# Performance work log

Measured on AMD Instinct MI355X. Metric: run time of the kernel, lower is better.

Reference implementation:

```python
import jax, jax.numpy as jnp
import numpy as np

B, L, H, E, V, T = 64, 512, 512, 512, 64, 200  # L must equal H (attention broadcast in source)
SOS_TOKEN = 0


def setup_inputs() -> dict:
    key = jax.random.key(0)
    ks = jax.random.split(key, 16)
    s = 0.05
    return {
        "seq_embeddings": jax.random.normal(ks[0], (B, L, H), jnp.float32),
        "key_w": jax.random.normal(ks[1], (H, H), jnp.float32) * s,
        "key_b": jax.random.normal(ks[2], (H,), jnp.float32) * s,
        "value_w": jax.random.normal(ks[3], (H, H), jnp.float32) * s,
        "value_b": jax.random.normal(ks[4], (H,), jnp.float32) * s,
        "char_emb": jax.random.normal(ks[5], (V, E), jnp.float32) * s,
        "w_ih": jax.random.normal(ks[6], (4 * H, E + H), jnp.float32) * s,
        "w_hh": jax.random.normal(ks[7], (4 * H, H), jnp.float32) * s,
        "b_ih": jax.random.normal(ks[8], (4 * H,), jnp.float32) * s,
        "b_hh": jax.random.normal(ks[9], (4 * H,), jnp.float32) * s,
        "cdn_w": jax.random.normal(ks[10], (V, 2 * H), jnp.float32) * s,
        "cdn_b": jax.random.normal(ks[11], (V,), jnp.float32) * s,
        "seq_embedding_lengths": jax.random.randint(ks[12], (B,), 1, L + 1),
        "batch_y": jax.random.randint(ks[13], (B, T), 0, V),
    }


def reference(seq_embeddings, key_w, key_b, value_w, value_b, char_emb,
              w_ih, w_hh, b_ih, b_hh, cdn_w, cdn_b,
              seq_embedding_lengths, batch_y):
    b, l, h = seq_embeddings.shape
    t = batch_y.shape[1]
    v = cdn_w.shape[0]
    dt = seq_embeddings.dtype

    # Attention: since logits = sum_l (keys*q) and context = sum_l (values*w),
    # both factor through the masked sum over L -> precompute once (loop-invariant).
    mask = (jnp.arange(l)[None, :] < seq_embedding_lengths[:, None]).astype(dt)  # (B, L)
    msum = jnp.einsum('blh,bl->bh', seq_embeddings, mask)                        # (B, H)
    keysum = msum @ key_w.T + l * key_b                                          # sum of keys over L
    valsum = msum @ value_w.T + l * value_b                                      # sum of values over L
    scale = jnp.sqrt(jnp.asarray(h, dt))

    def attend(q):  # q: (B, H); softmax over the key_dim axis, as in source
        w = jax.nn.softmax(keysum * q / scale, axis=1)
        return valsum * w

    ctx0 = attend(jnp.zeros((b, h), dt))
    h0 = jnp.zeros((b, h), dt)
    c0 = jnp.zeros((b, h), dt)

    # prev token at step i: SOS at i=1, batch_y[:, i-1] afterwards (tf_rate=1.0)
    prev_ys = jnp.concatenate(
        [jnp.full((1, b), SOS_TOKEN, dtype=batch_y.dtype), batch_y[:, 1:t - 1].T], axis=0)  # (T-1, B)

    def step(carry, y_prev):
        hh, cc, ctx = carry
        x = jnp.concatenate([char_emb[y_prev], ctx], axis=1)           # (B, E+H)
        gates = x @ w_ih.T + b_ih + hh @ w_hh.T + b_hh                 # (B, 4H)
        i_g, f_g, g_g, o_g = jnp.split(gates, 4, axis=1)
        cc = jax.nn.sigmoid(f_g) * cc + jax.nn.sigmoid(i_g) * jnp.tanh(g_g)
        hh = jax.nn.sigmoid(o_g) * jnp.tanh(cc)
        ctx = attend(hh)
        logit = jnp.concatenate([hh, ctx], axis=1) @ cdn_w.T + cdn_b   # (B, V)
        return (hh, cc, ctx), logit

    _, logits_seq = jax.lax.scan(step, (h0, c0, ctx0), prev_ys)        # (T-1, B, V)
    logits = jnp.concatenate(
        [jnp.zeros((1, b, v), dt), logits_seq], axis=0).transpose(1, 0, 2)  # (B, T, V)

    # multinomial sampling of output symbols (random in source; seeded here)
    samp = jax.random.categorical(jax.random.key(1), logits[:, 1:, :], axis=-1)
    symbols = jnp.concatenate(
        [jnp.zeros((b, 1), samp.dtype), samp], axis=1)                 # (B, T)
    return logits, symbols
```

## Files before the change

### kernel.cpp

```cpp
#include <hip/hip_runtime.h>
#include <math.h>

#define NB 64
#define NH 512
#define NV 64
#define NT 200
#define NSTEP 199
#define GBLK 256
#define GTHR 512

#define RLX   __ATOMIC_RELAXED
#define AGENT __HIP_MEMORY_SCOPE_AGENT
#define WGRP  __HIP_MEMORY_SCOPE_WORKGROUP

typedef float f4v __attribute__((ext_vector_type(4)));

__device__ inline float gumbel_tf(unsigned f){
  const unsigned ksc[3] = {0u, 1u, 0x1BD11BDBu};
  unsigned x0 = 0u + ksc[0];
  unsigned x1 = f  + ksc[1];
  const int R0[4] = {13,15,26,6};
  const int R1[4] = {17,29,16,24};
  #pragma unroll
  for (int i = 0; i < 5; ++i){
    #pragma unroll
    for (int r = 0; r < 4; ++r){
      int rot = (i & 1) ? R1[r] : R0[r];
      x0 += x1;
      x1 = (x1 << rot) | (x1 >> (32 - rot));
      x1 ^= x0;
    }
    x0 += ksc[(i+1)%3];
    x1 += ksc[(i+2)%3] + (unsigned)(i+1);
  }
  unsigned bits = x0 ^ x1;
  float u = __uint_as_float((bits >> 9) | 0x3F800000u) - 1.0f;
  u = fmaxf(u, 1.17549435e-38f);
  return -logf(-logf(u));
}

__device__ inline float sigf(float x){ return 1.0f/(1.0f + expf(-x)); }

__device__ inline void poll256(unsigned* flags, unsigned tgt){
  const int l = threadIdx.x & 63;
  #pragma unroll
  for (int j = 0; j < 4; ++j){
    while (__hip_atomic_load(&flags[(l*4 + j)*16], RLX, AGENT) < tgt){
      __builtin_amdgcn_s_sleep(1);
    }
  }
}
__device__ inline void poll64(unsigned* flags, unsigned tgt){
  const int l = threadIdx.x & 63;
  while (__hip_atomic_load(&flags[l*16], RLX, AGENT) < tgt){
    __builtin_amdgcn_s_sleep(1);
  }
}

__device__ inline float blk_red_max(float v, float* scr){
  #pragma unroll
  for (int m = 1; m < 64; m <<= 1) v = fmaxf(v, __shfl_xor(v, m, 64));
  if ((threadIdx.x & 63) == 0) scr[threadIdx.x >> 6] = v;
  __syncthreads();
  float r = scr[0];
  #pragma unroll
  for (int i = 1; i < 8; ++i) r = fmaxf(r, scr[i]);
  __syncthreads();
  return r;
}
__device__ inline float blk_red_sum(float v, float* scr){
  #pragma unroll
  for (int m = 1; m < 64; m <<= 1) v += __shfl_xor(v, m, 64);
  if ((threadIdx.x & 63) == 0) scr[threadIdx.x >> 6] = v;
  __syncthreads();
  float r = 0.f;
  #pragma unroll
  for (int i = 0; i < 8; ++i) r += scr[i];
  __syncthreads();
  return r;
}

__global__ void k_msum_part(const float* __restrict__ emb, const int* __restrict__ lens,
                            float* __restrict__ part){
  int blk = blockIdx.x, b = blk >> 3, lc = blk & 7;
  int len = lens[b];
  int l0 = lc*64, l1 = len < l0+64 ? len : l0+64;
  for (int h = threadIdx.x; h < 512; h += 256){
    float a = 0.f;
    for (int l = l0; l < l1; ++l) a += emb[(b*512 + l)*512 + h];
    part[blk*512 + h] = a;
  }
}
__global__ void k_msum(const float* __restrict__ part, float* __restrict__ msumT){
  int b = blockIdx.x;
  for (int h = threadIdx.x; h < 512; h += 256){
    float a = 0.f;
    #pragma unroll
    for (int lc = 0; lc < 8; ++lc) a += part[(b*8+lc)*512 + h];
    msumT[h*64 + b] = a;
  }
}
__global__ void k_kv(const float* __restrict__ msumT,
                     const float* __restrict__ kw, const float* __restrict__ kb,
                     const float* __restrict__ vw, const float* __restrict__ vb,
                     float* __restrict__ keysum, float* __restrict__ valsum){
  int which = blockIdx.x >> 7;
  int i = ((blockIdx.x & 127) << 2) + (threadIdx.x >> 6);
  int b = threadIdx.x & 63;
  const float* W = which ? vw : kw;
  float a = 0.f;
  for (int h = 0; h < 512; ++h) a = fmaf(msumT[h*64+b], W[i*512+h], a);
  float bias = which ? vb[i] : kb[i];
  float* out = which ? valsum : keysum;
  out[b*512 + i] = a + 512.0f*bias;
}
__global__ void k_ceT(const float* __restrict__ ce, float* __restrict__ ceT){
  int idx = blockIdx.x*256 + threadIdx.x;
  if (idx < 32768){ int v = idx >> 9, e = idx & 511; ceT[e*64 + v] = ce[v*512 + e]; }
}
__global__ void k_tok(const float* __restrict__ ceT, const float* __restrict__ w_ih,
                      const float* __restrict__ b_ih, const float* __restrict__ b_hh,
                      float* __restrict__ tok){
  int idx = blockIdx.x*256 + threadIdx.x;
  int v = idx & 63, row = idx >> 6;
  float a = 0.f;
  for (int e = 0; e < 512; ++e) a = fmaf(ceT[e*64+v], w_ih[row*1024 + e], a);
  tok[v*2048 + row] = a + b_ih[row] + b_hh[row];
}
__global__ void k_init(const float* __restrict__ valsum, const float* __restrict__ cdn_w,
                       float* __restrict__ cdnT, float* __restrict__ xT,
                       float* __restrict__ out, unsigned* __restrict__ bar){
  int idx = blockIdx.x*256 + threadIdx.x;
  if (idx < 65536){
    int v = idx >> 10, k = idx & 1023;
    cdnT[k*64 + v] = cdn_w[idx];
  } else if (idx < 98304){
    int r = idx - 65536; int j = r >> 6, b = r & 63;
    xT[j*64 + b] = valsum[b*512 + j] * (1.0f/512.0f);
  } else if (idx < 131072){
    xT[idx - 65536] = 0.f;
  } else if (idx < 135168){
    int r = idx - 131072; int b = r >> 6, v = r & 63;
    out[b*12800 + v] = 0.f;
  } else if (idx < 135232){
    int b = idx - 135168;
    out[819200 + b*200] = 0.f;
  } else if (idx < 139328){
    bar[idx - 135232] = 0u;
  }
}

__global__ __launch_bounds__(GTHR, 2) void k_loop(
    const float* __restrict__ w_ih, const float* __restrict__ w_hh,
    const int* __restrict__ batch_y, const float* __restrict__ tok,
    const float* __restrict__ keysum, const float* __restrict__ valsum,
    const float* __restrict__ cdnT, const float* __restrict__ cdn_b,
    float* __restrict__ xT, float* __restrict__ hT3, float* __restrict__ ctxT,
    float* __restrict__ out, unsigned* __restrict__ flags){
  __shared__ float W_lds[1024][8];
  __shared__ float red[8][8][64];
  __shared__ float gates_lds[8][64];
  __shared__ float cc_lds[2][64];
  __shared__ float pb_h[512], pb_c[512];
  __shared__ float pb_lp[8][64];
  __shared__ float scr[8];
  __shared__ int done_h, done_c, done_pb;

  const int tid = threadIdx.x;
  const int blk = blockIdx.x;
  const bool HASB = (blk < 64);
  const bool HASL = (blk >= 64 && blk < 128);

  if (tid == 0){ done_h = 0; done_c = 0; done_pb = 0; }
  for (int idx = tid; idx < 8192; idx += GTHR){
    int k = idx >> 3, r = idx & 7;
    int g = r >> 1, c = r & 1;
    int row = g*512 + blk*2 + c;
    W_lds[k][r] = (k < 512) ? w_ih[row*1024 + 512 + k] : w_hh[row*512 + (k - 512)];
  }
  if (tid < 128) cc_lds[tid >> 6][tid & 63] = 0.0f;
  __syncthreads();

  const int w = tid >> 6, l = tid & 63, kg = l >> 4, bg = l & 15;
  const float SCALE = 22.627416997969522f;

#define ISS1(R, JJ) do{ const float* _p = xin + (((kbase + (JJ)*4) << 6) | (bg << 2)); \
  asm volatile("global_load_dwordx4 %0, %1, off sc0 sc1" : "=v"(R) : "v"(_p)); }while(0)
#define ISS8(P, J0) do{ ISS1(P##0,(J0)+0);ISS1(P##1,(J0)+1);ISS1(P##2,(J0)+2);ISS1(P##3,(J0)+3); \
  ISS1(P##4,(J0)+4);ISS1(P##5,(J0)+5);ISS1(P##6,(J0)+6);ISS1(P##7,(J0)+7); }while(0)
#define CMP1(R, JJ) do{ int _k = kbase + (JJ)*4; \
  f4v _wA = *(const f4v*)&W_lds[_k][0]; f4v _wB = *(const f4v*)&W_lds[_k][4]; \
  float _wv[8] = {_wA.x,_wA.y,_wA.z,_wA.w,_wB.x,_wB.y,_wB.z,_wB.w}; \
  float _xv[4] = {R.x,R.y,R.z,R.w}; \
  _Pragma("unroll") for (int _r = 0; _r < 8; ++_r){ \
    _Pragma("unroll") for (int _q = 0; _q < 4; ++_q) \
      acc[_r][_q] = fmaf(_wv[_r], _xv[_q], acc[_r][_q]); } }while(0)
#define CMP8(P, J0) do{ CMP1(P##0,(J0)+0);CMP1(P##1,(J0)+1);CMP1(P##2,(J0)+2);CMP1(P##3,(J0)+3); \
  CMP1(P##4,(J0)+4);CMP1(P##5,(J0)+5);CMP1(P##6,(J0)+6);CMP1(P##7,(J0)+7); }while(0)
#define WAITV(N) do{ asm volatile("s_waitcnt vmcnt(" #N ")" ::: "memory"); \
  __builtin_amdgcn_sched_barrier(0); }while(0)

  for (int s = 0; s < NSTEP; ++s){
    const float* xin  = xT + (size_t)(s & 1)*65536;
    float*       xout = xT + (size_t)((s + 1) & 1)*65536;
    const unsigned t1 = (unsigned)(2*s + 1), t2 = (unsigned)(2*s + 2);
    const unsigned tgt_h = (s == 0) ? 0u : (unsigned)(2*s - 1);
    const unsigned tgt_c = (s == 0) ? 0u : (unsigned)(2*s);

    if (w >= 4){
      if (w == 4){
        poll256(flags, tgt_h);
        __hip_atomic_store(&done_h, s + 1, RLX, WGRP);
      } else {
        while (__hip_atomic_load(&done_h, RLX, WGRP) < s + 1) __builtin_amdgcn_s_sleep(1);
      }
    } else {
      if (w == 0){
        poll64(flags, tgt_c);
        __hip_atomic_store(&done_c, s + 1, RLX, WGRP);
      } else {
        while (__hip_atomic_load(&done_c, RLX, WGRP) < s + 1) __builtin_amdgcn_s_sleep(1);
      }
    }

    const int rr = tid >> 6, rb = tid & 63;
    int yprev = (s == 0) ? 0 : batch_y[rb*200 + s];
    float tokval = tok[yprev*2048 + (rr >> 1)*512 + blk*2 + (rr & 1)];

    float acc[8][4];
    #pragma unroll
    for (int r = 0; r < 8; ++r)
      #pragma unroll
      for (int q = 0; q < 4; ++q) acc[r][q] = 0.f;

    const int kbase = w*128 + kg;
    {
      f4v A0,A1,A2,A3,A4,A5,A6,A7,B0,B1,B2,B3,B4,B5,B6,B7;
      ISS8(A, 0);
      ISS8(B, 8);
      WAITV(8); CMP8(A, 0);
      ISS8(A, 16);
      WAITV(8); CMP8(B, 8);
      ISS8(B, 24);
      WAITV(8); CMP8(A, 16);
      WAITV(0); CMP8(B, 24);
    }

    #pragma unroll
    for (int r = 0; r < 8; ++r)
      #pragma unroll
      for (int q = 0; q < 4; ++q){
        float v = acc[r][q];
        v += __shfl_xor(v, 16, 64);
        v += __shfl_xor(v, 32, 64);
        acc[r][q] = v;
      }
    if (l < 16){
      #pragma unroll
      for (int r = 0; r < 8; ++r)
        *(float4*)&red[w][r][bg*4] = make_float4(acc[r][0], acc[r][1], acc[r][2], acc[r][3]);
    }
    __syncthreads();
    {
      float g = 0.f;
      #pragma unroll
      for (int ww = 0; ww < 8; ++ww) g += red[ww][rr][rb];
      gates_lds[rr][rb] = g + tokval;
    }
    __syncthreads();
    if (tid < 128){
      int c = tid >> 6, b = tid & 63;
      float ig = gates_lds[0 + c][b];
      float fg = gates_lds[2 + c][b];
      float gg = gates_lds[4 + c][b];
      float og = gates_lds[6 + c][b];
      float cprev = cc_lds[c][b];
      float cnew = sigf(fg)*cprev + sigf(ig)*tanhf(gg);
      float hnew = sigf(og)*tanhf(cnew);
      cc_lds[c][b] = cnew;
      float oldh = __hip_atomic_exchange(&xout[(512 + blk*2 + c)*64 + b], hnew, RLX, AGENT);
      asm volatile("" :: "v"(oldh));
      float oldt = __hip_atomic_exchange(
          &hT3[(size_t)((s + 1) % 3)*32768 + b*512 + (blk*2 + c)], hnew, RLX, AGENT);
      asm volatile("" :: "v"(oldt));
    }

    asm volatile("s_waitcnt vmcnt(0)" ::: "memory");
    __syncthreads();
    if (tid == 0){
      unsigned o = __hip_atomic_exchange(&flags[blk*16], HASB ? t1 : t2, RLX, AGENT);
      asm volatile("" :: "v"(o));
    }

    if (HASB){
      if (w == 4){
        poll256(flags, t1);
        __hip_atomic_store(&done_pb, s + 1, RLX, WGRP);
      } else {
        while (__hip_atomic_load(&done_pb, RLX, WGRP) < s + 1) __builtin_amdgcn_s_sleep(1);
      }

      int b = blk;
      int jj = tid;
      float h;
      { const float* hp = hT3 + (size_t)((s + 1) % 3)*32768 + b*512 + jj;
        asm volatile("global_load_dword %0, %1, off sc0 sc1" : "=v"(h) : "v"(hp));
        asm volatile("s_waitcnt vmcnt(0)" ::: "memory"); }
      pb_h[jj] = h;
      float sc = (keysum[b*512 + jj] * h) / SCALE;
      float m = blk_red_max(sc, scr);
      float e = expf(sc - m);
      float S = blk_red_sum(e, scr);
      float cx = valsum[b*512 + jj] * (e / S);
      float oldc = __hip_atomic_exchange(&xout[jj*64 + b], cx, RLX, AGENT);
      asm volatile("" :: "v"(oldc));
      float oldt = __hip_atomic_exchange(&ctxT[(size_t)(s & 1)*32768 + b*512 + jj], cx, RLX, AGENT);
      asm volatile("" :: "v"(oldt));
      asm volatile("s_waitcnt vmcnt(0)" ::: "memory");
      __syncthreads();
      if (tid == 0){
        unsigned o = __hip_atomic_exchange(&flags[blk*16], t2, RLX, AGENT);
        asm volatile("" :: "v"(o));
      }
    }

    if (HASL && s >= 1){
      int b = blk - 64;
      int sp = s - 1;
      float h, c;
      { const float* hp = hT3 + (size_t)(s % 3)*32768 + b*512 + tid;
        const float* cp = ctxT + (size_t)(sp & 1)*32768 + b*512 + tid;
        asm volatile("global_load_dword %0, %1, off sc0 sc1" : "=v"(h) : "v"(hp));
        asm volatile("global_load_dword %0, %1, off sc0 sc1" : "=v"(c) : "v"(cp));
        asm volatile("s_waitcnt vmcnt(0)" ::: "memory"); }
      pb_h[tid] = h;
      pb_c[tid] = c;
      __syncthreads();
      int kq = tid >> 6, v = tid & 63;
      float part = 0.f;
      for (int k = kq*128; k < kq*128 + 128; ++k){
        float xh = (k < 512) ? pb_h[k] : pb_c[k - 512];
        part = fmaf(cdnT[k*64 + v], xh, part);
      }
      pb_lp[kq][v] = part;
      __syncthreads();
      if (tid < 64){
        int v2 = tid;
        float logit = cdn_b[v2];
        #pragma unroll
        for (int q = 0; q < 8; ++q) logit += pb_lp[q][v2];
        out[b*12800 + (sp+1)*64 + v2] = logit;
        float z = gumbel_tf((unsigned)((b*199 + sp)*64 + v2)) + logit;
        int idx = v2;
        #pragma unroll
        for (int mm = 1; mm < 64; mm <<= 1){
          float oz = __shfl_xor(z, mm, 64);
          int   oi = __shfl_xor(idx, mm, 64);
          if (oz > z || (oz == z && oi < idx)){ z = oz; idx = oi; }
        }
        if (v2 == 0) out[819200 + b*200 + (sp+1)] = (float)idx;
      }
    }
  }

  if (HASL){
    int b = blk - 64;
    const int sp = NSTEP - 1;
    if (tid == 0){
      while (__hip_atomic_load(&flags[b*16], RLX, AGENT) < (unsigned)(2*sp + 2))
        __builtin_amdgcn_s_sleep(1);
    }
    __syncthreads();
    float h, c;
    { const float* hp = hT3 + (size_t)((sp + 1) % 3)*32768 + b*512 + tid;
      const float* cp = ctxT + (size_t)(sp & 1)*32768 + b*512 + tid;
      asm volatile("global_load_dword %0, %1, off sc0 sc1" : "=v"(h) : "v"(hp));
      asm volatile("global_load_dword %0, %1, off sc0 sc1" : "=v"(c) : "v"(cp));
      asm volatile("s_waitcnt vmcnt(0)" ::: "memory"); }
    pb_h[tid] = h;
    pb_c[tid] = c;
    __syncthreads();
    int kq = tid >> 6, v = tid & 63;
    float part = 0.f;
    for (int k = kq*128; k < kq*128 + 128; ++k){
      float xh = (k < 512) ? pb_h[k] : pb_c[k - 512];
      part = fmaf(cdnT[k*64 + v], xh, part);
    }
    pb_lp[kq][v] = part;
    __syncthreads();
    if (tid < 64){
      int v2 = tid;
      float logit = cdn_b[v2];
      #pragma unroll
      for (int q = 0; q < 8; ++q) logit += pb_lp[q][v2];
      out[b*12800 + (sp+1)*64 + v2] = logit;
      float z = gumbel_tf((unsigned)((b*199 + sp)*64 + v2)) + logit;
      int idx = v2;
      #pragma unroll
      for (int mm = 1; mm < 64; mm <<= 1){
        float oz = __shfl_xor(z, mm, 64);
        int   oi = __shfl_xor(idx, mm, 64);
        if (oz > z || (oz == z && oi < idx)){ z = oz; idx = oi; }
      }
      if (v2 == 0) out[819200 + b*200 + (sp+1)] = (float)idx;
    }
  }
#undef ISS1
#undef ISS8
#undef CMP1
#undef CMP8
#undef WAITV
}

extern "C" void kernel_launch(void* const* d_in, const int* in_sizes, int n_in,
                              void* d_out, int out_size, void* d_ws, size_t ws_size,
                              hipStream_t stream){
  const float* seq     = (const float*)d_in[0];
  const float* key_w   = (const float*)d_in[1];
  const float* key_b   = (const float*)d_in[2];
  const float* value_w = (const float*)d_in[3];
  const float* value_b = (const float*)d_in[4];
  const float* char_e  = (const float*)d_in[5];
  const float* w_ih    = (const float*)d_in[6];
  const float* w_hh    = (const float*)d_in[7];
  const float* b_ih    = (const float*)d_in[8];
  const float* b_hh    = (const float*)d_in[9];
  const float* cdn_w   = (const float*)d_in[10];
  const float* cdn_b   = (const float*)d_in[11];
  const int*   lens    = (const int*)d_in[12];
  const int*   batch_y = (const int*)d_in[13];
  float* out = (float*)d_out;
  float* ws  = (float*)d_ws;

  float* hT3       = ws;
  float* ctxT      = ws + 98304;
  float* msum_part = ws;
  float* msumT     = ws + 262144;
  float* keysum    = ws + 294912;
  float* valsum    = ws + 327680;
  float* tok       = ws + 360448;
  float* cdnT      = ws + 491520;
  float* ceT       = ws + 557056;
  float* xT        = ws + 589824;
  unsigned* bar    = (unsigned*)(ws + 720896);

  k_msum_part<<<512, 256, 0, stream>>>(seq, lens, msum_part);
  k_msum     <<<64,  256, 0, stream>>>(msum_part, msumT);
  k_kv       <<<256, 256, 0, stream>>>(msumT, key_w, key_b, value_w, value_b, keysum, valsum);
  k_ceT      <<<128, 256, 0, stream>>>(char_e, ceT);
  k_tok      <<<512, 256, 0, stream>>>(ceT, w_ih, b_ih, b_hh, tok);
  k_init     <<<545, 256, 0, stream>>>(valsum, cdn_w, cdnT, xT, out, bar);

  k_loop<<<GBLK, GTHR, 0, stream>>>(w_ih, w_hh, batch_y, tok, keysum, valsum,
                                    cdnT, cdn_b, xT, hT3, ctxT, out, bar);
  (void)in_sizes; (void)n_in; (void)out_size; (void)ws_size;
}
```

Before: 4.811 ms.

## Recompute attention context from broadcast softmax max/sum instead of materializing ctx

The attention blocks now publish only the per-batch softmax max and sum rather than writing the full 512-wide context vector into xT and a separate ctx buffer. Consumers (the gate GEMM warps for the ctx half and the logit blocks) recompute the context on the fly from h, transposed keysum/valsum and the published max/sum. This removes the per-step global scatter of ctx and shortens the critical path between attention and the next step. In exchange it adds redundant exp/div work and extra keysum/valsum loads in every block, plus a new pipelined load loop.

New measurement: 16.37 ms. 240% more time.

```diff
diff --git a/kernel.cpp b/kernel.cpp
--- a/kernel.cpp
+++ b/kernel.cpp
@@ -127,8 +127,10 @@
   for (int e = 0; e < 512; ++e) a = fmaf(ceT[e*64+v], w_ih[row*1024 + e], a);
   tok[v*2048 + row] = a + b_ih[row] + b_hh[row];
 }
-__global__ void k_init(const float* __restrict__ valsum, const float* __restrict__ cdn_w,
+__global__ void k_init(const float* __restrict__ keysum, const float* __restrict__ valsum,
+                       const float* __restrict__ cdn_w,
                        float* __restrict__ cdnT, float* __restrict__ xT,
+                       float* __restrict__ ksT, float* __restrict__ vsT,
                        float* __restrict__ out, unsigned* __restrict__ bar){
   int idx = blockIdx.x*256 + threadIdx.x;
   if (idx < 65536){
@@ -147,6 +149,12 @@
     out[819200 + b*200] = 0.f;
   } else if (idx < 139328){
     bar[idx - 135232] = 0u;
+  } else if (idx < 172096){
+    int r = idx - 139328; int j = r >> 6, b = r & 63;
+    ksT[j*64 + b] = keysum[b*512 + j];
+  } else if (idx < 204864){
+    int r = idx - 172096; int j = r >> 6, b = r & 63;
+    vsT[j*64 + b] = valsum[b*512 + j];
   }
 }
 
@@ -155,7 +163,8 @@
     const int* __restrict__ batch_y, const float* __restrict__ tok,
     const float* __restrict__ keysum, const float* __restrict__ valsum,
     const float* __restrict__ cdnT, const float* __restrict__ cdn_b,
-    float* __restrict__ xT, float* __restrict__ hT3, float* __restrict__ ctxT,
+    const float* __restrict__ ksT, const float* __restrict__ vsT,
+    float* __restrict__ mS, float* __restrict__ xT, float* __restrict__ hT3,
     float* __restrict__ out, unsigned* __restrict__ flags){
   __shared__ float W_lds[1024][8];
   __shared__ float red[8][8][64];
@@ -188,15 +197,15 @@
   asm volatile("global_load_dwordx4 %0, %1, off sc0 sc1" : "=v"(R) : "v"(_p)); }while(0)
 #define ISS8(P, J0) do{ ISS1(P##0,(J0)+0);ISS1(P##1,(J0)+1);ISS1(P##2,(J0)+2);ISS1(P##3,(J0)+3); \
   ISS1(P##4,(J0)+4);ISS1(P##5,(J0)+5);ISS1(P##6,(J0)+6);ISS1(P##7,(J0)+7); }while(0)
-#define CMP1(R, JJ) do{ int _k = kbase + (JJ)*4; \
+#define CMPX(R, JJ) do{ int _k = kbase + (JJ)*4; \
   f4v _wA = *(const f4v*)&W_lds[_k][0]; f4v _wB = *(const f4v*)&W_lds[_k][4]; \
   float _wv[8] = {_wA.x,_wA.y,_wA.z,_wA.w,_wB.x,_wB.y,_wB.z,_wB.w}; \
   float _xv[4] = {R.x,R.y,R.z,R.w}; \
   _Pragma("unroll") for (int _r = 0; _r < 8; ++_r){ \
     _Pragma("unroll") for (int _q = 0; _q < 4; ++_q) \
       acc[_r][_q] = fmaf(_wv[_r], _xv[_q], acc[_r][_q]); } }while(0)
-#define CMP8(P, J0) do{ CMP1(P##0,(J0)+0);CMP1(P##1,(J0)+1);CMP1(P##2,(J0)+2);CMP1(P##3,(J0)+3); \
-  CMP1(P##4,(J0)+4);CMP1(P##5,(J0)+5);CMP1(P##6,(J0)+6);CMP1(P##7,(J0)+7); }while(0)
+#define CMP8(P, J0) do{ CMPX(P##0,(J0)+0);CMPX(P##1,(J0)+1);CMPX(P##2,(J0)+2);CMPX(P##3,(J0)+3); \
+  CMPX(P##4,(J0)+4);CMPX(P##5,(J0)+5);CMPX(P##6,(J0)+6);CMPX(P##7,(J0)+7); }while(0)
 #define WAITV(N) do{ asm volatile("s_waitcnt vmcnt(" #N ")" ::: "memory"); \
   __builtin_amdgcn_sched_barrier(0); }while(0)
 
@@ -234,7 +243,7 @@
       for (int q = 0; q < 4; ++q) acc[r][q] = 0.f;
 
     const int kbase = w*128 + kg;
-    {
+    if (w >= 4 || s == 0){
       f4v A0,A1,A2,A3,A4,A5,A6,A7,B0,B1,B2,B3,B4,B5,B6,B7;
       ISS8(A, 0);
       ISS8(B, 8);
@@ -244,6 +253,45 @@
       ISS8(B, 24);
       WAITV(8); CMP8(A, 16);
       WAITV(0); CMP8(B, 24);
+    } else {
+      f4v m4, S4;
+      { const float* _mp = mS + (size_t)(s & 1)*128 + (bg << 2);
+        asm volatile("global_load_dwordx4 %0, %1, off sc0 sc1" : "=v"(m4) : "v"(_mp));
+        const float* _sp2 = _mp + 64;
+        asm volatile("global_load_dwordx4 %0, %1, off sc0 sc1" : "=v"(S4) : "v"(_sp2)); }
+      f4v xv[4], kv[4], vv[4];
+      #pragma unroll
+      for (int jj = 0; jj < 4; ++jj){
+        int k = kbase + jj*4;
+        const float* hp = xin + (((512 + k) << 6) | (bg << 2));
+        const float* kp = ksT + ((k << 6) | (bg << 2));
+        const float* vp = vsT + ((k << 6) | (bg << 2));
+        asm volatile("global_load_dwordx4 %0, %1, off sc0 sc1" : "=v"(xv[jj]) : "v"(hp));
+        asm volatile("global_load_dwordx4 %0, %1, off" : "=v"(kv[jj]) : "v"(kp));
+        asm volatile("global_load_dwordx4 %0, %1, off" : "=v"(vv[jj]) : "v"(vp));
+      }
+      WAITV(12);
+      #pragma unroll
+      for (int jj = 0; jj < 32; ++jj){
+        if (jj <= 28) WAITV(9); else if (jj == 29) WAITV(6); else if (jj == 30) WAITV(3); else WAITV(0);
+        const int bank = jj & 3;
+        f4v h4 = xv[bank], k4 = kv[bank], v4 = vv[bank];
+        f4v cx4;
+        { float sc0 = (k4.x*h4.x)/SCALE; float e0 = expf(sc0 - m4.x); cx4.x = v4.x*(e0/S4.x);
+          float sc1 = (k4.y*h4.y)/SCALE; float e1 = expf(sc1 - m4.y); cx4.y = v4.y*(e1/S4.y);
+          float sc2 = (k4.z*h4.z)/SCALE; float e2 = expf(sc2 - m4.z); cx4.z = v4.z*(e2/S4.z);
+          float sc3 = (k4.w*h4.w)/SCALE; float e3 = expf(sc3 - m4.w); cx4.w = v4.w*(e3/S4.w); }
+        CMPX(cx4, jj);
+        if (jj < 28){
+          int k = kbase + (jj + 4)*4;
+          const float* hp = xin + (((512 + k) << 6) | (bg << 2));
+          const float* kp = ksT + ((k << 6) | (bg << 2));
+          const float* vp = vsT + ((k << 6) | (bg << 2));
+          asm volatile("global_load_dwordx4 %0, %1, off sc0 sc1" : "=v"(xv[bank]) : "v"(hp));
+          asm volatile("global_load_dwordx4 %0, %1, off" : "=v"(kv[bank]) : "v"(kp));
+          asm volatile("global_load_dwordx4 %0, %1, off" : "=v"(vv[bank]) : "v"(vp));
+        }
+      }
     }
 
     #pragma unroll
@@ -306,16 +354,18 @@
       { const float* hp = hT3 + (size_t)((s + 1) % 3)*32768 + b*512 + jj;
         asm volatile("global_load_dword %0, %1, off sc0 sc1" : "=v"(h) : "v"(hp));
         asm volatile("s_waitcnt vmcnt(0)" ::: "memory"); }
-      pb_h[jj] = h;
       float sc = (keysum[b*512 + jj] * h) / SCALE;
       float m = blk_red_max(sc, scr);
       float e = expf(sc - m);
       float S = blk_red_sum(e, scr);
-      float cx = valsum[b*512 + jj] * (e / S);
-      float oldc = __hip_atomic_exchange(&xout[jj*64 + b], cx, RLX, AGENT);
-      asm volatile("" :: "v"(oldc));
-      float oldt = __hip_atomic_exchange(&ctxT[(size_t)(s & 1)*32768 + b*512 + jj], cx, RLX, AGENT);
-      asm volatile("" :: "v"(oldt));
+      float* mp = mS + (size_t)((s + 1) & 1)*128;
+      if (tid == 0){
+        float o = __hip_atomic_exchange(&mp[b], m, RLX, AGENT);
+        asm volatile("" :: "v"(o));
+      } else if (tid == 1){
+        float o = __hip_atomic_exchange(&mp[64 + b], S, RLX, AGENT);
+        asm volatile("" :: "v"(o));
+      }
       asm volatile("s_waitcnt vmcnt(0)" ::: "memory");
       __syncthreads();
       if (tid == 0){
@@ -327,12 +377,17 @@
     if (HASL && s >= 1){
       int b = blk - 64;
       int sp = s - 1;
-      float h, c;
+      float h, mm, SS;
       { const float* hp = hT3 + (size_t)(s % 3)*32768 + b*512 + tid;
-        const float* cp = ctxT + (size_t)(sp & 1)*32768 + b*512 + tid;
-        asm volatile("global_load_dword %0, %1, off sc0 sc1" : "=v"(h) : "v"(hp));
-        asm volatile("global_load_dword %0, %1, off sc0 sc1" : "=v"(c) : "v"(cp));
+        const float* mp = mS + (size_t)(s & 1)*128 + b;
+        const float* sp2 = mp + 64;
+        asm volatile("global_load_dword %0, %1, off sc0 sc1" : "=v"(h)  : "v"(hp));
+        asm volatile("global_load_dword %0, %1, off sc0 sc1" : "=v"(mm) : "v"(mp));
+        asm volatile("global_load_dword %0, %1, off sc0 sc1" : "=v"(SS) : "v"(sp2));
         asm volatile("s_waitcnt vmcnt(0)" ::: "memory"); }
+      float sc = (keysum[b*512 + tid] * h) / SCALE;
+      float e = expf(sc - mm);
+      float c = valsum[b*512 + tid] * (e / SS);
       pb_h[tid] = h;
       pb_c[tid] = c;
       __syncthreads();
@@ -353,9 +408,9 @@
         float z = gumbel_tf((unsigned)((b*199 + sp)*64 + v2)) + logit;
         int idx = v2;
         #pragma unroll
-        for (int mm = 1; mm < 64; mm <<= 1){
-          float oz = __shfl_xor(z, mm, 64);
-          int   oi = __shfl_xor(idx, mm, 64);
+        for (int mm2 = 1; mm2 < 64; mm2 <<= 1){
+          float oz = __shfl_xor(z, mm2, 64);
+          int   oi = __shfl_xor(idx, mm2, 64);
           if (oz > z || (oz == z && oi < idx)){ z = oz; idx = oi; }
         }
         if (v2 == 0) out[819200 + b*200 + (sp+1)] = (float)idx;
@@ -371,12 +426,17 @@
         __builtin_amdgcn_s_sleep(1);
     }
     __syncthreads();
-    float h, c;
+    float h, mm, SS;
     { const float* hp = hT3 + (size_t)((sp + 1) % 3)*32768 + b*512 + tid;
-      const float* cp = ctxT + (size_t)(sp & 1)*32768 + b*512 + tid;
-      asm volatile("global_load_dword %0, %1, off sc0 sc1" : "=v"(h) : "v"(hp));
-      asm volatile("global_load_dword %0, %1, off sc0 sc1" : "=v"(c) : "v"(cp));
+      const float* mp = mS + (size_t)((sp + 1) & 1)*128 + b;
+      const float* sp2 = mp + 64;
+      asm volatile("global_load_dword %0, %1, off sc0 sc1" : "=v"(h)  : "v"(hp));
+      asm volatile("global_load_dword %0, %1, off sc0 sc1" : "=v"(mm) : "v"(mp));
+      asm volatile("global_load_dword %0, %1, off sc0 sc1" : "=v"(SS) : "v"(sp2));
       asm volatile("s_waitcnt vmcnt(0)" ::: "memory"); }
+    float sc = (keysum[b*512 + tid] * h) / SCALE;
+    float e = expf(sc - mm);
+    float c = valsum[b*512 + tid] * (e / SS);
     pb_h[tid] = h;
     pb_c[tid] = c;
     __syncthreads();
@@ -397,9 +457,9 @@
       float z = gumbel_tf((unsigned)((b*199 + sp)*64 + v2)) + logit;
       int idx = v2;
       #pragma unroll
-      for (int mm = 1; mm < 64; mm <<= 1){
-        float oz = __shfl_xor(z, mm, 64);
-        int   oi = __shfl_xor(idx, mm, 64);
+      for (int mm2 = 1; mm2 < 64; mm2 <<= 1){
+        float oz = __shfl_xor(z, mm2, 64);
+        int   oi = __shfl_xor(idx, mm2, 64);
         if (oz > z || (oz == z && oi < idx)){ z = oz; idx = oi; }
       }
       if (v2 == 0) out[819200 + b*200 + (sp+1)] = (float)idx;
@@ -407,7 +467,7 @@
   }
 #undef ISS1
 #undef ISS8
-#undef CMP1
+#undef CMPX
 #undef CMP8
 #undef WAITV
 }
@@ -433,7 +493,9 @@
   float* ws  = (float*)d_ws;
 
   float* hT3       = ws;
-  float* ctxT      = ws + 98304;
+  float* ksT       = ws + 98304;
+  float* vsT       = ws + 131072;
+  float* mS        = ws + 163840;
   float* msum_part = ws;
   float* msumT     = ws + 262144;
   float* keysum    = ws + 294912;
@@ -449,9 +511,9 @@
   k_kv       <<<256, 256, 0, stream>>>(msumT, key_w, key_b, value_w, value_b, keysum, valsum);
   k_ceT      <<<128, 256, 0, stream>>>(char_e, ceT);
   k_tok      <<<512, 256, 0, stream>>>(ceT, w_ih, b_ih, b_hh, tok);
-  k_init     <<<545, 256, 0, stream>>>(valsum, cdn_w, cdnT, xT, out, bar);
+  k_init     <<<801, 256, 0, stream>>>(keysum, valsum, cdn_w, cdnT, xT, ksT, vsT, out, bar);
 
   k_loop<<<GBLK, GTHR, 0, stream>>>(w_ih, w_hh, batch_y, tok, keysum, valsum,
-                                    cdnT, cdn_b, xT, hT3, ctxT, out, bar);
+                                    cdnT, cdn_b, ksT, vsT, mS, xT, hT3, out, bar);
   (void)in_sizes; (void)n_in; (void)out_size; (void)ws_size;
 }
```

## Mirror context half of x per XCC into local L2 copies for cached loads

Applied to the files above, without the earlier changes.

Blocks on each XCC (except XCC 7) cooperatively copy the context half of the shared x buffer into a per-XCC workspace chunk each step. The gate matvec then reads it with L2-cacheable loads instead of system-coherent loads. New cross-block counters per XCC (copy done, reads done) synchronise the copy and its reuse. The separate ctxT buffer is dropped, and the logits path reads context directly from xT. This adds extra copy traffic and extra per-step synchronisation across blocks in the serial loop.

Result: slower. 5.385 ms (+11.9%).

```diff
diff --git a/kernel.cpp b/kernel.cpp
--- a/kernel.cpp
+++ b/kernel.cpp
@@ -155,7 +155,7 @@
     const int* __restrict__ batch_y, const float* __restrict__ tok,
     const float* __restrict__ keysum, const float* __restrict__ valsum,
     const float* __restrict__ cdnT, const float* __restrict__ cdn_b,
-    float* __restrict__ xT, float* __restrict__ hT3, float* __restrict__ ctxT,
+    float* __restrict__ xT, float* __restrict__ hT3, float* __restrict__ wsb,
     float* __restrict__ out, unsigned* __restrict__ flags){
   __shared__ float W_lds[1024][8];
   __shared__ float red[8][8][64];
@@ -164,14 +164,29 @@
   __shared__ float pb_h[512], pb_c[512];
   __shared__ float pb_lp[8][64];
   __shared__ float scr[8];
-  __shared__ int done_h, done_c, done_pb;
+  __shared__ int done_h, done_c, done_pb, done_m;
+  __shared__ int cpy_done, myrank_s;
 
   const int tid = threadIdx.x;
   const int blk = blockIdx.x;
   const bool HASB = (blk < 64);
   const bool HASL = (blk >= 64 && blk < 128);
 
-  if (tid == 0){ done_h = 0; done_c = 0; done_pb = 0; }
+  unsigned xcc = 0;
+  asm("s_getreg_b32 %0, hwreg(HW_REG_XCC_ID)" : "=s"(xcc));
+  xcc &= 7u;
+  const bool MIR = (xcc < 7u);
+  unsigned* xcnt  = &flags[xcc*512 + 8];
+  unsigned* xdone = &flags[xcc*512 + 136];
+  unsigned* xread = &flags[xcc*512 + 264];
+  const unsigned moff[7] = {98304u,131072u,163840u,196608u,229376u,262144u,557056u};
+  float* mchunk = wsb + (MIR ? moff[xcc] : 0u);
+
+  if (tid == 0){
+    done_h = 0; done_c = 0; done_pb = 0; done_m = 0; cpy_done = 0;
+    unsigned r = __hip_atomic_fetch_add(xcnt, 1u, RLX, AGENT);
+    myrank_s = (int)r;
+  }
   for (int idx = tid; idx < 8192; idx += GTHR){
     int k = idx >> 3, r = idx & 7;
     int g = r >> 1, c = r & 1;
@@ -180,23 +195,28 @@
   }
   if (tid < 128) cc_lds[tid >> 6][tid & 63] = 0.0f;
   __syncthreads();
+  const int myrank = myrank_s;
 
   const int w = tid >> 6, l = tid & 63, kg = l >> 4, bg = l & 15;
   const float SCALE = 22.627416997969522f;
 
-#define ISS1(R, JJ) do{ const float* _p = xin + (((kbase + (JJ)*4) << 6) | (bg << 2)); \
+#define ISSC(R, JJ) do{ const float* _p = xin + (((kbase + (JJ)*4) << 6) | (bg << 2)); \
   asm volatile("global_load_dwordx4 %0, %1, off sc0 sc1" : "=v"(R) : "v"(_p)); }while(0)
-#define ISS8(P, J0) do{ ISS1(P##0,(J0)+0);ISS1(P##1,(J0)+1);ISS1(P##2,(J0)+2);ISS1(P##3,(J0)+3); \
-  ISS1(P##4,(J0)+4);ISS1(P##5,(J0)+5);ISS1(P##6,(J0)+6);ISS1(P##7,(J0)+7); }while(0)
-#define CMP1(R, JJ) do{ int _k = kbase + (JJ)*4; \
+#define ISSM(R, JJ) do{ const float* _p = mchunk + (((kbase + (JJ)*4) << 6) | (bg << 2)); \
+  asm volatile("global_load_dwordx4 %0, %1, off sc0" : "=v"(R) : "v"(_p)); }while(0)
+#define ISSC8(P, J0) do{ ISSC(P##0,(J0)+0);ISSC(P##1,(J0)+1);ISSC(P##2,(J0)+2);ISSC(P##3,(J0)+3); \
+  ISSC(P##4,(J0)+4);ISSC(P##5,(J0)+5);ISSC(P##6,(J0)+6);ISSC(P##7,(J0)+7); }while(0)
+#define ISSM8(P, J0) do{ ISSM(P##0,(J0)+0);ISSM(P##1,(J0)+1);ISSM(P##2,(J0)+2);ISSM(P##3,(J0)+3); \
+  ISSM(P##4,(J0)+4);ISSM(P##5,(J0)+5);ISSM(P##6,(J0)+6);ISSM(P##7,(J0)+7); }while(0)
+#define CMPX(R, JJ) do{ int _k = kbase + (JJ)*4; \
   f4v _wA = *(const f4v*)&W_lds[_k][0]; f4v _wB = *(const f4v*)&W_lds[_k][4]; \
   float _wv[8] = {_wA.x,_wA.y,_wA.z,_wA.w,_wB.x,_wB.y,_wB.z,_wB.w}; \
   float _xv[4] = {R.x,R.y,R.z,R.w}; \
   _Pragma("unroll") for (int _r = 0; _r < 8; ++_r){ \
     _Pragma("unroll") for (int _q = 0; _q < 4; ++_q) \
       acc[_r][_q] = fmaf(_wv[_r], _xv[_q], acc[_r][_q]); } }while(0)
-#define CMP8(P, J0) do{ CMP1(P##0,(J0)+0);CMP1(P##1,(J0)+1);CMP1(P##2,(J0)+2);CMP1(P##3,(J0)+3); \
-  CMP1(P##4,(J0)+4);CMP1(P##5,(J0)+5);CMP1(P##6,(J0)+6);CMP1(P##7,(J0)+7); }while(0)
+#define CMP8(P, J0) do{ CMPX(P##0,(J0)+0);CMPX(P##1,(J0)+1);CMPX(P##2,(J0)+2);CMPX(P##3,(J0)+3); \
+  CMPX(P##4,(J0)+4);CMPX(P##5,(J0)+5);CMPX(P##6,(J0)+6);CMPX(P##7,(J0)+7); }while(0)
 #define WAITV(N) do{ asm volatile("s_waitcnt vmcnt(" #N ")" ::: "memory"); \
   __builtin_amdgcn_sched_barrier(0); }while(0)
 
@@ -217,9 +237,41 @@
     } else {
       if (w == 0){
         poll64(flags, tgt_c);
+        if (MIR && s > 0){
+          unsigned need = (unsigned)(s - 1) * __hip_atomic_load(xcnt, RLX, AGENT);
+          while (__hip_atomic_load(xread, RLX, AGENT) < need) __builtin_amdgcn_s_sleep(1);
+        }
         __hip_atomic_store(&done_c, s + 1, RLX, WGRP);
       } else {
         while (__hip_atomic_load(&done_c, RLX, WGRP) < s + 1) __builtin_amdgcn_s_sleep(1);
+      }
+      if (MIR && s > 0){
+        unsigned Rv = __hip_atomic_load(xcnt, RLX, AGENT);
+        unsigned t256 = (unsigned)((w << 6) | l);
+        for (unsigned idx = (unsigned)myrank*256u + t256; idx < 8192u; idx += Rv*256u){
+          f4v tmp;
+          const float* sp = xin + (size_t)idx*4u;
+          asm volatile("global_load_dwordx4 %0, %1, off sc0 sc1" : "=v"(tmp) : "v"(sp));
+          asm volatile("s_waitcnt vmcnt(0)" ::: "memory");
+          *(f4v*)(mchunk + (size_t)idx*4u) = tmp;
+        }
+        asm volatile("s_waitcnt vmcnt(0)" ::: "memory");
+        if (l == 0){
+          int o = __hip_atomic_fetch_add(&cpy_done, 1, RLX, WGRP);
+          asm volatile("" :: "v"(o));
+        }
+        if (w == 0){
+          if (l == 0){
+            while (__hip_atomic_load(&cpy_done, RLX, WGRP) < 4*s) __builtin_amdgcn_s_sleep(1);
+            unsigned o = __hip_atomic_fetch_add(xdone, 1u, RLX, AGENT);
+            asm volatile("" :: "v"(o));
+            unsigned need = (unsigned)s * Rv;
+            while (__hip_atomic_load(xdone, RLX, AGENT) < need) __builtin_amdgcn_s_sleep(1);
+          }
+          __hip_atomic_store(&done_m, s + 1, RLX, WGRP);
+        } else {
+          while (__hip_atomic_load(&done_m, RLX, WGRP) < s + 1) __builtin_amdgcn_s_sleep(1);
+        }
       }
     }
 
@@ -234,14 +286,24 @@
       for (int q = 0; q < 4; ++q) acc[r][q] = 0.f;
 
     const int kbase = w*128 + kg;
-    {
+    if (w < 4 && s > 0 && MIR){
       f4v A0,A1,A2,A3,A4,A5,A6,A7,B0,B1,B2,B3,B4,B5,B6,B7;
-      ISS8(A, 0);
-      ISS8(B, 8);
+      ISSM8(A, 0);
+      ISSM8(B, 8);
       WAITV(8); CMP8(A, 0);
-      ISS8(A, 16);
+      ISSM8(A, 16);
       WAITV(8); CMP8(B, 8);
-      ISS8(B, 24);
+      ISSM8(B, 24);
+      WAITV(8); CMP8(A, 16);
+      WAITV(0); CMP8(B, 24);
+    } else {
+      f4v A0,A1,A2,A3,A4,A5,A6,A7,B0,B1,B2,B3,B4,B5,B6,B7;
+      ISSC8(A, 0);
+      ISSC8(B, 8);
+      WAITV(8); CMP8(A, 0);
+      ISSC8(A, 16);
+      WAITV(8); CMP8(B, 8);
+      ISSC8(B, 24);
       WAITV(8); CMP8(A, 16);
       WAITV(0); CMP8(B, 24);
     }
@@ -261,6 +323,10 @@
         *(float4*)&red[w][r][bg*4] = make_float4(acc[r][0], acc[r][1], acc[r][2], acc[r][3]);
     }
     __syncthreads();
+    if (tid == 0 && MIR && s > 0){
+      unsigned o = __hip_atomic_fetch_add(xread, 1u, RLX, AGENT);
+      asm volatile("" :: "v"(o));
+    }
     {
       float g = 0.f;
       #pragma unroll
@@ -314,8 +380,6 @@
       float cx = valsum[b*512 + jj] * (e / S);
       float oldc = __hip_atomic_exchange(&xout[jj*64 + b], cx, RLX, AGENT);
       asm volatile("" :: "v"(oldc));
-      float oldt = __hip_atomic_exchange(&ctxT[(size_t)(s & 1)*32768 + b*512 + jj], cx, RLX, AGENT);
-      asm volatile("" :: "v"(oldt));
       asm volatile("s_waitcnt vmcnt(0)" ::: "memory");
       __syncthreads();
       if (tid == 0){
@@ -329,7 +393,7 @@
       int sp = s - 1;
       float h, c;
       { const float* hp = hT3 + (size_t)(s % 3)*32768 + b*512 + tid;
-        const float* cp = ctxT + (size_t)(sp & 1)*32768 + b*512 + tid;
+        const float* cp = xT + (size_t)(s & 1)*65536 + tid*64 + b;
         asm volatile("global_load_dword %0, %1, off sc0 sc1" : "=v"(h) : "v"(hp));
         asm volatile("global_load_dword %0, %1, off sc0 sc1" : "=v"(c) : "v"(cp));
         asm volatile("s_waitcnt vmcnt(0)" ::: "memory"); }
@@ -373,7 +437,7 @@
     __syncthreads();
     float h, c;
     { const float* hp = hT3 + (size_t)((sp + 1) % 3)*32768 + b*512 + tid;
-      const float* cp = ctxT + (size_t)(sp & 1)*32768 + b*512 + tid;
+      const float* cp = xT + (size_t)((sp + 1) & 1)*65536 + tid*64 + b;
       asm volatile("global_load_dword %0, %1, off sc0 sc1" : "=v"(h) : "v"(hp));
       asm volatile("global_load_dword %0, %1, off sc0 sc1" : "=v"(c) : "v"(cp));
       asm volatile("s_waitcnt vmcnt(0)" ::: "memory"); }
@@ -405,9 +469,11 @@
       if (v2 == 0) out[819200 + b*200 + (sp+1)] = (float)idx;
     }
   }
-#undef ISS1
-#undef ISS8
-#undef CMP1
+#undef ISSC
+#undef ISSM
+#undef ISSC8
+#undef ISSM8
+#undef CMPX
 #undef CMP8
 #undef WAITV
 }
@@ -433,7 +499,6 @@
   float* ws  = (float*)d_ws;
 
   float* hT3       = ws;
-  float* ctxT      = ws + 98304;
   float* msum_part = ws;
   float* msumT     = ws + 262144;
   float* keysum    = ws + 294912;
@@ -452,6 +517,6 @@
   k_init     <<<545, 256, 0, stream>>>(valsum, cdn_w, cdnT, xT, out, bar);
 
   k_loop<<<GBLK, GTHR, 0, stream>>>(w_ih, w_hh, batch_y, tok, keysum, valsum,
-                                    cdnT, cdn_b, xT, hT3, ctxT, out, bar);
+                                    cdnT, cdn_b, xT, hT3, ws, out, bar);
   (void)in_sizes; (void)n_in; (void)out_size; (void)ws_size;
 }
```

## Spread flag polling across waves and drop redundant ctx buffer writes

Applied to the files above, without the earlier changes.

Each of waves 0-3 now polls the 64 gate flags itself instead of relaying through an LDS done counter. The attention phase spreads its 256-flag poll across the first 32 lanes of every wave, followed by a block barrier, instead of one wave polling and the rest spinning on LDS. The separate ctxT buffer and its per-step atomic store are removed; the logit blocks read context directly from the transposed xT buffer. The aim is shorter cross-block synchronization latency and one fewer global atomic per element per step, at the cost of more concurrent global polling traffic and strided context reads.

After: 4.929 ms. 1.02x slower.

```diff
diff --git a/kernel.cpp b/kernel.cpp
--- a/kernel.cpp
+++ b/kernel.cpp
@@ -155,7 +155,7 @@
     const int* __restrict__ batch_y, const float* __restrict__ tok,
     const float* __restrict__ keysum, const float* __restrict__ valsum,
     const float* __restrict__ cdnT, const float* __restrict__ cdn_b,
-    float* __restrict__ xT, float* __restrict__ hT3, float* __restrict__ ctxT,
+    float* __restrict__ xT, float* __restrict__ hT3,
     float* __restrict__ out, unsigned* __restrict__ flags){
   __shared__ float W_lds[1024][8];
   __shared__ float red[8][8][64];
@@ -164,14 +164,14 @@
   __shared__ float pb_h[512], pb_c[512];
   __shared__ float pb_lp[8][64];
   __shared__ float scr[8];
-  __shared__ int done_h, done_c, done_pb;
+  __shared__ int done_h;
 
   const int tid = threadIdx.x;
   const int blk = blockIdx.x;
   const bool HASB = (blk < 64);
   const bool HASL = (blk >= 64 && blk < 128);
 
-  if (tid == 0){ done_h = 0; done_c = 0; done_pb = 0; }
+  if (tid == 0){ done_h = 0; }
   for (int idx = tid; idx < 8192; idx += GTHR){
     int k = idx >> 3, r = idx & 7;
     int g = r >> 1, c = r & 1;
@@ -188,15 +188,15 @@
   asm volatile("global_load_dwordx4 %0, %1, off sc0 sc1" : "=v"(R) : "v"(_p)); }while(0)
 #define ISS8(P, J0) do{ ISS1(P##0,(J0)+0);ISS1(P##1,(J0)+1);ISS1(P##2,(J0)+2);ISS1(P##3,(J0)+3); \
   ISS1(P##4,(J0)+4);ISS1(P##5,(J0)+5);ISS1(P##6,(J0)+6);ISS1(P##7,(J0)+7); }while(0)
-#define CMP1(R, JJ) do{ int _k = kbase + (JJ)*4; \
+#define CMPX(R, JJ) do{ int _k = kbase + (JJ)*4; \
   f4v _wA = *(const f4v*)&W_lds[_k][0]; f4v _wB = *(const f4v*)&W_lds[_k][4]; \
   float _wv[8] = {_wA.x,_wA.y,_wA.z,_wA.w,_wB.x,_wB.y,_wB.z,_wB.w}; \
   float _xv[4] = {R.x,R.y,R.z,R.w}; \
   _Pragma("unroll") for (int _r = 0; _r < 8; ++_r){ \
     _Pragma("unroll") for (int _q = 0; _q < 4; ++_q) \
       acc[_r][_q] = fmaf(_wv[_r], _xv[_q], acc[_r][_q]); } }while(0)
-#define CMP8(P, J0) do{ CMP1(P##0,(J0)+0);CMP1(P##1,(J0)+1);CMP1(P##2,(J0)+2);CMP1(P##3,(J0)+3); \
-  CMP1(P##4,(J0)+4);CMP1(P##5,(J0)+5);CMP1(P##6,(J0)+6);CMP1(P##7,(J0)+7); }while(0)
+#define CMP8(P, J0) do{ CMPX(P##0,(J0)+0);CMPX(P##1,(J0)+1);CMPX(P##2,(J0)+2);CMPX(P##3,(J0)+3); \
+  CMPX(P##4,(J0)+4);CMPX(P##5,(J0)+5);CMPX(P##6,(J0)+6);CMPX(P##7,(J0)+7); }while(0)
 #define WAITV(N) do{ asm volatile("s_waitcnt vmcnt(" #N ")" ::: "memory"); \
   __builtin_amdgcn_sched_barrier(0); }while(0)
 
@@ -215,12 +215,7 @@
         while (__hip_atomic_load(&done_h, RLX, WGRP) < s + 1) __builtin_amdgcn_s_sleep(1);
       }
     } else {
-      if (w == 0){
-        poll64(flags, tgt_c);
-        __hip_atomic_store(&done_c, s + 1, RLX, WGRP);
-      } else {
-        while (__hip_atomic_load(&done_c, RLX, WGRP) < s + 1) __builtin_amdgcn_s_sleep(1);
-      }
+      poll64(flags, tgt_c);
     }
 
     const int rr = tid >> 6, rb = tid & 63;
@@ -293,12 +288,13 @@
     }
 
     if (HASB){
-      if (w == 4){
-        poll256(flags, t1);
-        __hip_atomic_store(&done_pb, s + 1, RLX, WGRP);
-      } else {
-        while (__hip_atomic_load(&done_pb, RLX, WGRP) < s + 1) __builtin_amdgcn_s_sleep(1);
-      }
+      if (l < 32){
+        unsigned fidx = (unsigned)((w*32 + l)*16);
+        while (__hip_atomic_load(&flags[fidx], RLX, AGENT) < t1){
+          __builtin_amdgcn_s_sleep(1);
+        }
+      }
+      __syncthreads();
 
       int b = blk;
       int jj = tid;
@@ -314,8 +310,6 @@
       float cx = valsum[b*512 + jj] * (e / S);
       float oldc = __hip_atomic_exchange(&xout[jj*64 + b], cx, RLX, AGENT);
       asm volatile("" :: "v"(oldc));
-      float oldt = __hip_atomic_exchange(&ctxT[(size_t)(s & 1)*32768 + b*512 + jj], cx, RLX, AGENT);
-      asm volatile("" :: "v"(oldt));
       asm volatile("s_waitcnt vmcnt(0)" ::: "memory");
       __syncthreads();
       if (tid == 0){
@@ -329,7 +323,7 @@
       int sp = s - 1;
       float h, c;
       { const float* hp = hT3 + (size_t)(s % 3)*32768 + b*512 + tid;
-        const float* cp = ctxT + (size_t)(sp & 1)*32768 + b*512 + tid;
+        const float* cp = xT + (size_t)(s & 1)*65536 + tid*64 + b;
         asm volatile("global_load_dword %0, %1, off sc0 sc1" : "=v"(h) : "v"(hp));
         asm volatile("global_load_dword %0, %1, off sc0 sc1" : "=v"(c) : "v"(cp));
         asm volatile("s_waitcnt vmcnt(0)" ::: "memory"); }
@@ -373,7 +367,7 @@
     __syncthreads();
     float h, c;
     { const float* hp = hT3 + (size_t)((sp + 1) % 3)*32768 + b*512 + tid;
-      const float* cp = ctxT + (size_t)(sp & 1)*32768 + b*512 + tid;
+      const float* cp = xT + (size_t)((sp + 1) & 1)*65536 + tid*64 + b;
       asm volatile("global_load_dword %0, %1, off sc0 sc1" : "=v"(h) : "v"(hp));
       asm volatile("global_load_dword %0, %1, off sc0 sc1" : "=v"(c) : "v"(cp));
       asm volatile("s_waitcnt vmcnt(0)" ::: "memory"); }
@@ -407,7 +401,7 @@
   }
 #undef ISS1
 #undef ISS8
-#undef CMP1
+#undef CMPX
 #undef CMP8
 #undef WAITV
 }
@@ -433,7 +427,6 @@
   float* ws  = (float*)d_ws;
 
   float* hT3       = ws;
-  float* ctxT      = ws + 98304;
   float* msum_part = ws;
   float* msumT     = ws + 262144;
   float* keysum    = ws + 294912;
@@ -452,6 +445,6 @@
   k_init     <<<545, 256, 0, stream>>>(valsum, cdn_w, cdnT, xT, out, bar);
 
   k_loop<<<GBLK, GTHR, 0, stream>>>(w_ih, w_hh, batch_y, tok, keysum, valsum,
-                                    cdnT, cdn_b, xT, hT3, ctxT, out, bar);
+                                    cdnT, cdn_b, xT, hT3, out, bar);
   (void)in_sizes; (void)n_in; (void)out_size; (void)ws_size;
 }
```
